# Performance work log

Hardware: AMD Instinct MI355X
Metric: run time of the kernel (lower is better)

## Reference

```python
import jax, jax.numpy as jnp
import numpy as np

B, S, L, H, E, V = 32, 48, 48, 1024, 1024, 32000


def setup_inputs() -> dict:
    key = jax.random.key(0)
    ks = jax.random.split(key, 16)
    s = 0.02
    return {
        "label": jax.random.randint(ks[0], (B, S), 0, V),
        "init_hidden": jax.random.normal(ks[1], (1, B, H), jnp.float32),
        "encoder_output": jax.random.normal(ks[2], (B, L, H), jnp.float32),
        "emb": jax.random.normal(ks[3], (V, E), jnp.float32) * s,
        "attn_W": jax.random.normal(ks[4], (2 * H, L), jnp.float32) * s,
        "attn_b": jnp.zeros((L,), jnp.float32),
        "comb_W": jax.random.normal(ks[5], (2 * H, H), jnp.float32) * s,
        "comb_b": jnp.zeros((H,), jnp.float32),
        "W_ih": jax.random.normal(ks[6], (E, 3 * H), jnp.float32) * s,
        "W_hh": jax.random.normal(ks[7], (H, 3 * H), jnp.float32) * s,
        "b_ih": jnp.zeros((3 * H,), jnp.float32),
        "b_hh": jnp.zeros((3 * H,), jnp.float32),
        "out_W": jax.random.normal(ks[8], (H, V), jnp.float32) * s,
        "out_b": jnp.zeros((V,), jnp.float32),
    }


def _decode(label, init_hidden, encoder_output, emb, attn_W, attn_b,
            comb_W, comb_b, W_ih, W_hh, b_ih, b_hh, out_W, out_b):
    # Teacher forcing (teaching_force_rate=1.0): inputs are relu(embedding(label[:, i]))
    xs = jax.nn.relu(emb[label])            # (B, S, E)
    xs = jnp.transpose(xs, (1, 0, 2))       # (S, B, E) for scan

    def step(h, xe):                        # h: (B,H), xe: (B,E)
        # Attention: Linear(cat(emb, hidden)) -> nn.Softmax() on a 3D (B,1,L)
        # tensor, which in torch defaults to dim=0 (the batch dim) -- replicated.
        sim = jnp.concatenate([xe, h], axis=-1) @ attn_W + attn_b   # (B, L)
        w = jax.nn.softmax(sim, axis=0)                             # over batch (faithful)
        ctx = jnp.einsum('bl,blh->bh', w, encoder_output)           # bmm
        g = jax.nn.relu(jnp.concatenate([ctx, xe], axis=-1) @ comb_W + comb_b)  # (B,H)
        # Single GRU step (torch gate order: r, z, n)
        gx = g @ W_ih + b_ih
        gh = h @ W_hh + b_hh
        xr, xz, xn = jnp.split(gx, 3, axis=-1)
        hr, hz, hn = jnp.split(gh, 3, axis=-1)
        r = jax.nn.sigmoid(xr + hr)
        z = jax.nn.sigmoid(xz + hz)
        n = jnp.tanh(xn + r * hn)
        h_new = (1.0 - z) * n + z * h
        out = jax.nn.log_softmax(h_new @ out_W + out_b, axis=-1)    # (B, V)
        return h_new, out

    _, outs = jax.lax.scan(step, init_hidden[0], xs)   # outs: (S, B, V)
    return jnp.transpose(outs, (1, 0, 2))              # (B, S, V)


def reference(label, init_hidden, encoder_output, emb, attn_W, attn_b,
              comb_W, comb_b, W_ih, W_hh, b_ih, b_hh, out_W, out_b):
    return _decode(label, init_hidden, encoder_output, emb, attn_W, attn_b,
                   comb_W, comb_b, W_ih, W_hh, b_ih, b_hh, out_W, out_b)
```

## Files before the change

### kernel.cpp

```cpp
#include <hip/hip_runtime.h>

#define NB 32
#define NS 48
#define NL 48
#define NH 1024
#define NE 1024
#define NV 32000
#define NR (NS*NB)
#define K3H 3072
#define RA_BLOCKS 64
#define RB_BLOCKS 128
#define RC_BLOCKS 64
#define NBLK_FULL (RA_BLOCKS + RB_BLOCKS + RC_BLOCKS)

typedef unsigned short u16;
typedef __bf16 bf16x8 __attribute__((ext_vector_type(8)));
typedef unsigned short ushort8 __attribute__((ext_vector_type(8)));
typedef float f32x4 __attribute__((ext_vector_type(4)));
typedef unsigned int uint4v __attribute__((ext_vector_type(4)));

__device__ __forceinline__ float bf2f(u16 x) {
    union { unsigned u; float f; } c; c.u = ((unsigned)x) << 16; return c.f;
}
__device__ __forceinline__ u16 f2bf(float f) {
    union { float f; unsigned u; } c; c.f = f;
    unsigned r = (c.u + 0x7FFFu + ((c.u >> 16) & 1u)) >> 16;
    return (u16)r;
}
__device__ __forceinline__ f32x4 mfma16(bf16x8 a, bf16x8 b, f32x4 c) {
    return __builtin_amdgcn_mfma_f32_16x16x32_bf16(a, b, c, 0, 0, 0);
}
__device__ __forceinline__ void gld_lds16(const void* g, void* l) {
    __builtin_amdgcn_global_load_lds((const __attribute__((address_space(1))) void*)g,
                                     (__attribute__((address_space(3))) void*)l, 16, 0, 0);
}

__device__ __forceinline__ void st16_coh(void* p, uint4v v) {
    asm volatile("global_store_dwordx4 %0, %1, off sc0 sc1" :: "v"(p), "v"(v) : "memory");
}
__device__ __forceinline__ void waitb(const int* line, int tgt) {
    if (tgt <= 0) return;
    int guard = 0; int v;
    for (;;) {
        asm volatile("global_load_dword %0, %1, off sc0 sc1\n\ts_waitcnt vmcnt(0)"
                     : "=v"(v) : "v"(line) : "memory");
        if (v >= tgt) return;
        __builtin_amdgcn_s_sleep(1);
        if (++guard > (1 << 20)) return;
    }
}
__device__ __forceinline__ void arrive2(int* cnt, int* superc, int* bcast, int lineMask, int val) {
    asm volatile("s_waitcnt vmcnt(0)" ::: "memory");
    int prev = __hip_atomic_fetch_add(cnt, 1, __ATOMIC_RELAXED, __HIP_MEMORY_SCOPE_AGENT);
    if ((prev & lineMask) == lineMask) {
        int p2 = __hip_atomic_fetch_add(superc, 1, __ATOMIC_RELAXED, __HIP_MEMORY_SCOPE_AGENT);
        if ((p2 & 7) == 7) {
#pragma unroll
            for (int i = 0; i < 24; ++i)
                asm volatile("global_store_dword %0, %1, off sc0 sc1"
                             :: "v"(bcast + i * 64), "v"(val) : "memory");
        }
    }
}

__global__ __launch_bounds__(256) void transpose_cast(const float* __restrict__ src, int K, int N,
                                                      char* __restrict__ dst, int bf16out) {
    __shared__ float tile[32][33];
    int k0 = blockIdx.y * 32, n0 = blockIdx.x * 32;
    int tx = threadIdx.x & 31, ty = threadIdx.x >> 5;
    for (int i = 0; i < 4; ++i) {
        int n = n0 + tx;
        float v = (n < N) ? src[(size_t)(k0 + ty + i*8) * N + n] : 0.f;
        tile[ty + i*8][tx] = v;
    }
    __syncthreads();
    for (int i = 0; i < 4; ++i) {
        int n = n0 + ty + i*8;
        int k = k0 + tx;
        if (n < N) {
            float v = tile[tx][ty + i*8];
            if (bf16out) ((u16*)dst)[(size_t)n * K + k] = f2bf(v);
            else         ((float*)dst)[(size_t)n * K + k] = v;
        }
    }
}

__global__ __launch_bounds__(256) void prep_inputs(const int* __restrict__ label, const float* __restrict__ emb,
                                                   const float* __restrict__ enc, const float* __restrict__ inith,
                                                   u16* __restrict__ xe, u16* __restrict__ encb, u16* __restrict__ hallx) {
    int blk = blockIdx.x, t = threadIdx.x;
    if (blk < NR) {
        int s = blk >> 5, b = blk & 31;
        int lab = label[b * NS + s];
        const float* src = emb + (size_t)lab * NE;
        u16* dst = xe + (size_t)blk * NE;
        for (int i = t; i < NE; i += 256) { float v = src[i]; dst[i] = f2bf(v > 0.f ? v : 0.f); }
    } else if (blk < 2 * NR) {
        int r = blk - NR;
        const float* src = enc + (size_t)r * NH;
        u16* dst = encb + (size_t)r * NH;
        for (int i = t; i < NH; i += 256) dst[i] = f2bf(src[i]);
    } else {
        int b = blk - 2 * NR;
        const float* src = inith + (size_t)b * NH;
        u16* dst = hallx + (size_t)b * NH;
        for (int i = t; i < NH; i += 256) dst[i] = f2bf(src[i]);
    }
}

__global__ __launch_bounds__(384) void simxe2_kernel(const u16* __restrict__ xe, const u16* __restrict__ aw1t,
                                                     const float* __restrict__ attnB, float* __restrict__ simxe) {
    int r = blockIdx.x, t = threadIdx.x;
    int l = t >> 3, part = t & 7;
    const u16* x = xe + (size_t)r * 1024 + part * 128;
    const u16* ww = aw1t + (size_t)l * 1024 + part * 128;
    float acc = 0.f;
#pragma unroll
    for (int k = 0; k < 128; k += 8) {
        ushort8 xv = *reinterpret_cast<const ushort8*>(x + k);
        ushort8 wv = *reinterpret_cast<const ushort8*>(ww + k);
#pragma unroll
        for (int u = 0; u < 8; ++u) acc += bf2f(xv[u]) * bf2f(wv[u]);
    }
    acc += __shfl_xor(acc, 1);
    acc += __shfl_xor(acc, 2);
    acc += __shfl_xor(acc, 4);
    if (part == 0) simxe[(size_t)r * NL + l] = acc + attnB[l];
}

template<int MODE>
__global__ __launch_bounds__(256) void gemm_bf16(const u16* __restrict__ A, const u16* __restrict__ Bt,
                                                 void* __restrict__ Cout, const float* __restrict__ bias, int N) {
    __shared__ u16 ldsA[128 * 64];
    __shared__ u16 ldsB[128 * 64];
    const int t = threadIdx.x;
    const int lane = t & 63, w = t >> 6;
    const int wm = w >> 1, wn = w & 1;
    const int m0 = blockIdx.x * 128, n0 = blockIdx.y * 128;
    f32x4 acc[4][4] = {};
    for (int kt = 0; kt < 16; ++kt) {
        const int k0 = kt * 64;
#pragma unroll
        for (int i = 0; i < 4; ++i) {
            int chunk = i * 256 + t;
            int row = chunk >> 3, slot = chunk & 7;
            int srck = ((slot ^ (row & 7)) * 8);
            const u16* ga = A  + (size_t)(m0 + row) * 1024 + k0 + srck;
            const u16* gb = Bt + (size_t)(n0 + row) * 1024 + k0 + srck;
            u16* la = ldsA + (size_t)(i * 256 + w * 64) * 8;
            u16* lb = ldsB + (size_t)(i * 256 + w * 64) * 8;
            gld_lds16(ga, la);
            gld_lds16(gb, lb);
        }
        asm volatile("s_waitcnt vmcnt(0)" ::: "memory");
        __syncthreads();
#pragma unroll
        for (int kk = 0; kk < 2; ++kk) {
            bf16x8 a[4], b[4];
#pragma unroll
            for (int f = 0; f < 4; ++f) {
                int rowA = wm * 64 + f * 16 + (lane & 15);
                int slotA = (kk * 4 + (lane >> 4)) ^ (rowA & 7);
                a[f] = *reinterpret_cast<const bf16x8*>(ldsA + rowA * 64 + slotA * 8);
                int rowB = wn * 64 + f * 16 + (lane & 15);
                int slotB = (kk * 4 + (lane >> 4)) ^ (rowB & 7);
                b[f] = *reinterpret_cast<const bf16x8*>(ldsB + rowB * 64 + slotB * 8);
            }
#pragma unroll
            for (int fm = 0; fm < 4; ++fm)
#pragma unroll
                for (int fn = 0; fn < 4; ++fn)
                    acc[fm][fn] = mfma16(a[fm], b[fn], acc[fm][fn]);
        }
        __syncthreads();
    }
#pragma unroll
    for (int fm = 0; fm < 4; ++fm) {
#pragma unroll
        for (int fn = 0; fn < 4; ++fn) {
#pragma unroll
            for (int rr = 0; rr < 4; ++rr) {
                int m = m0 + wm * 64 + fm * 16 + (lane >> 4) * 4 + rr;
                int n = n0 + wn * 64 + fn * 16 + (lane & 15);
                float v = acc[fm][fn][rr];
                if (bias) v += bias[n];
                if (MODE == 0)      ((float*)Cout)[(size_t)m * N + n] = v;
                else if (MODE == 2) ((u16*)Cout)[(size_t)m * N + n] = f2bf(v);
                else if (MODE == 1)
                    ((float*)Cout)[((size_t)(m & 31) * NS + (m >> 5)) * NV + n] = v;
                else
                    ((u16*)Cout)[((size_t)(m & 31) * NS + (m >> 5)) * NV + n] = f2bf(v);
            }
        }
    }
}

__device__ __forceinline__ void do_tile256(char* smem, const u16* Ab, const u16* outWT,
                                           const float* outB, u16* logit,
                                           int mt, int nt, int t) {
    u16* ldsA = (u16*)smem;
    u16* ldsB = (u16*)(smem + 32768);
    const int w = t >> 6, lane = t & 63;
    const int r16 = lane & 15, kg = lane >> 4;
    const int wm = w >> 1, wn = w & 1;
    const int m0 = mt * 256, n0 = nt * 128;
    f32x4 acc[4][4] = {};
    for (int kt = 0; kt < 16; ++kt) {
        const int k0 = kt * 64;
#pragma unroll
        for (int i = 0; i < 4; ++i) {
            int chunk = i * 512 + t;
            int row = chunk >> 3, slot = chunk & 7;
            int srck = ((slot ^ (row & 7)) * 8);
            gld_lds16(Ab + (size_t)(m0 + row) * 1024 + k0 + srck,
                      ldsA + (size_t)(i * 512 + w * 64) * 8);
        }
#pragma unroll
        for (int i = 0; i < 2; ++i) {
            int chunk = i * 512 + t;
            int row = chunk >> 3, slot = chunk & 7;
            int srck = ((slot ^ (row & 7)) * 8);
            gld_lds16(outWT + (size_t)(n0 + row) * 1024 + k0 + srck,
                      ldsB + (size_t)(i * 512 + w * 64) * 8);
        }
        asm volatile("s_waitcnt vmcnt(0)" ::: "memory");
        __syncthreads();
#pragma unroll
        for (int kk = 0; kk < 2; ++kk) {
            bf16x8 a[4], b[4];
#pragma unroll
            for (int f = 0; f < 4; ++f) {
                int rowA = wm * 64 + f * 16 + r16;
                int slotA = (kk * 4 + kg) ^ (rowA & 7);
                a[f] = *reinterpret_cast<const bf16x8*>(ldsA + rowA * 64 + slotA * 8);
                int rowB = wn * 64 + f * 16 + r16;
                int slotB = (kk * 4 + kg) ^ (rowB & 7);
                b[f] = *reinterpret_cast<const bf16x8*>(ldsB + rowB * 64 + slotB * 8);
            }
#pragma unroll
            for (int fm = 0; fm < 4; ++fm)
#pragma unroll
                for (int fn = 0; fn < 4; ++fn)
                    acc[fm][fn] = mfma16(a[fm], b[fn], acc[fm][fn]);
        }
        __syncthreads();
    }
#pragma unroll
    for (int fm = 0; fm < 4; ++fm) {
#pragma unroll
        for (int fn = 0; fn < 4; ++fn) {
#pragma unroll
            for (int rr = 0; rr < 4; ++rr) {
                int m = m0 + wm * 64 + fm * 16 + kg * 4 + rr;
                int n = n0 + wn * 64 + fn * 16 + r16;
                float v = acc[fm][fn][rr] + outB[n];
                logit[((size_t)(m & 31) * NS + (m >> 5)) * NV + n] = f2bf(v);
            }
        }
    }
}

__device__ __forceinline__ void queue_gemm(char* smem, int* qslot, int* qcnt,
                                           const u16* Ab, const u16* outWT,
                                           const float* outB, u16* logit, int t) {
    for (;;) {
        __syncthreads();
        if (t == 0) *qslot = __hip_atomic_fetch_add(qcnt, 1, __ATOMIC_RELAXED, __HIP_MEMORY_SCOPE_AGENT);
        __syncthreads();
        int nt = *qslot;
        if (nt >= 250) return;
        do_tile256(smem, Ab, outWT, outB, logit, 5, nt, t);
    }
}

__global__ __launch_bounds__(512) void recurrence9(
    const float* __restrict__ simxe, const u16* __restrict__ gxe,
    const u16* __restrict__ P, const u16* __restrict__ aw2t,
    const u16* __restrict__ whht, const u16* __restrict__ wiht,
    const float* __restrict__ b_ih, const float* __restrict__ b_hh,
    u16* __restrict__ g_rot, u16* __restrict__ hallx,
    const float* __restrict__ outW, const float* __restrict__ outB,
    u16* __restrict__ outWT, u16* __restrict__ logit, int* __restrict__ bar, int fused)
{
    __shared__ __align__(16) char smem[155776];
    int* cntA   = bar;
    int* cntB   = bar + 512;
    int* superA = bar + 1024;
    int* superB = bar + 1088;
    int* bcastA = bar + 1152;
    int* bcastB = bar + 2688;
    int* cntC   = bar + 4224;
    int* qcnt   = bar + 4288;
    int* qslot  = (int*)(smem + 153600);
    const int blk = blockIdx.x, t = threadIdx.x;
    const int lane = t & 63, w = t >> 6;
    const int r16 = lane & 15, kg = lane >> 4;
    const u16* Ab = hallx + NB * NH;

    if (blk < RA_BLOCKS) {
        int* myB = bcastB + (blk % 24) * 64;
        const int b = blk >> 1, half = blk & 1;
        u16*   W2T  = (u16*)smem;
        u16*   Pl   = (u16*)(smem + 99072);
        float* siml = (float*)(smem + 148224);
        float* wl   = (float*)(smem + 154496);
        u16*   gtmp = (u16*)(smem + 154752);
        for (int idx = t; idx < 48 * 1024; idx += 512) {
            int l = idx >> 10, k = idx & 1023;
            W2T[l * 1032 + k] = aw2t[idx];
        }
        for (int idx = t; idx < 48 * 512; idx += 512) {
            int l = idx >> 9, j = idx & 511;
            Pl[idx] = P[((size_t)(b * 48 + l)) * NH + half * 512 + j];
        }
        __syncthreads();
        const int mt = w & 1, nt = w >> 1;
        const int m0 = mt * 16, n0 = nt * 16;

        for (int s = 0; s < NS; ++s) {
            float gxev = bf2f(gxe[((size_t)(s * 32 + b)) * NH + half * 512 + t]);
            float sxv0 = 0.f, sxv1 = 0.f, sxv2 = 0.f, sxv3 = 0.f;
            if (w < 6) {
                const float* sxe = simxe + (size_t)(s * 32) * NL;
                sxv0 = sxe[(m0 + kg * 4 + 0) * NL + n0 + r16];
                sxv1 = sxe[(m0 + kg * 4 + 1) * NL + n0 + r16];
                sxv2 = sxe[(m0 + kg * 4 + 2) * NL + n0 + r16];
                sxv3 = sxe[(m0 + kg * 4 + 3) * NL + n0 + r16];
            }
            if (t == 0) waitb(myB, s);
            __syncthreads();
            const u16* hprev = hallx + (size_t)s * (NB * NH);
            if (w < 6) {
                f32x4 acc0; f32x4 acc1 = {};
                acc0[0] = sxv0; acc0[1] = sxv1; acc0[2] = sxv2; acc0[3] = sxv3;
                const u16* aP = hprev + (size_t)(m0 + r16) * NH + kg * 8;
                const u16* bP = W2T + (n0 + r16) * 1032 + kg * 8;
#pragma unroll
                for (int k = 0; k < 1024; k += 64) {
                    acc0 = mfma16(*reinterpret_cast<const bf16x8*>(aP + k),
                                  *reinterpret_cast<const bf16x8*>(bP + k), acc0);
                    acc1 = mfma16(*reinterpret_cast<const bf16x8*>(aP + k + 32),
                                  *reinterpret_cast<const bf16x8*>(bP + k + 32), acc1);
                }
#pragma unroll
                for (int rr = 0; rr < 4; ++rr)
                    siml[(m0 + kg * 4 + rr) * 49 + n0 + r16] = acc0[rr] + acc1[rr];
            }
            __syncthreads();
            if (t < 384) {
                int l = t >> 3, p = t & 7;
                float v0 = siml[(p * 4 + 0) * 49 + l];
                float v1 = siml[(p * 4 + 1) * 49 + l];
                float v2 = siml[(p * 4 + 2) * 49 + l];
                float v3 = siml[(p * 4 + 3) * 49 + l];
                float m = fmaxf(fmaxf(v0, v1), fmaxf(v2, v3));
                m = fmaxf(m, __shfl_xor(m, 1));
                m = fmaxf(m, __shfl_xor(m, 2));
                m = fmaxf(m, __shfl_xor(m, 4));
                float den = __expf(v0 - m) + __expf(v1 - m) + __expf(v2 - m) + __expf(v3 - m);
                den += __shfl_xor(den, 1);
                den += __shfl_xor(den, 2);
                den += __shfl_xor(den, 4);
                if (p == (b >> 2)) {
                    int bi = b & 3;
                    float vb = bi == 0 ? v0 : bi == 1 ? v1 : bi == 2 ? v2 : v3;
                    wl[l] = __expf(vb - m) / den;
                }
            }
            __syncthreads();
            {
                float acc = gxev;
#pragma unroll
                for (int l = 0; l < 48; ++l) acc += wl[l] * bf2f(Pl[l * 512 + t]);
                gtmp[t] = f2bf(fmaxf(acc, 0.f));
            }
            __syncthreads();
            if (t < 64) {
                uint4v v = *reinterpret_cast<const uint4v*>(gtmp + t * 8);
                st16_coh(g_rot + (size_t)s * (NB * NH) + (size_t)b * NH + half * 512 + t * 8, v);
            }
            if (t == 0) arrive2(cntA + (blk & 7) * 64, superA, bcastA, 7, s + 1);
        }
        if (fused) {
            if (t == 0) { waitb(myB, 48); waitb(cntC, RC_BLOCKS); }
            __syncthreads();
            queue_gemm(smem, qslot, qcnt, Ab, outWT, outB, logit, t);
        }
    } else if (blk < RA_BLOCKS + RB_BLOCKS) {
        const int rb = blk - RA_BLOCKS;
        int* myB = bcastB + (rb % 24) * 64;
        int* myA = bcastA + (rb % 24) * 64;
        const int c0 = rb * 8;
        u16*   Whh = (u16*)smem;
        u16*   Wih = (u16*)(smem + 66048);
        float* ghs = (float*)(smem + 132096);
        float* gxs = (float*)(smem + 140288);
        u16*   htmp = (u16*)(smem + 148480);
        for (int idx = t; idx < 32 * 1024; idx += 512) {
            int pr = idx >> 10, k = idx & 1023;
            u16 vh = 0, vi = 0;
            if (pr < 24) {
                size_t srow = (size_t)((pr >> 3) * 1024 + c0 + (pr & 7));
                vh = whht[srow * NH + k];
                vi = wiht[srow * NH + k];
            }
            Whh[pr * 1032 + k] = vh;
            Wih[pr * 1032 + k] = vi;
        }
        const int gb2 = (t & 255) >> 3, gcol = t & 7;
        const float bxr = b_ih[c0 + gcol], bxz = b_ih[1024 + c0 + gcol], bxn = b_ih[2048 + c0 + gcol];
        const float bhr = b_hh[c0 + gcol], bhz = b_hh[1024 + c0 + gcol], bhn = b_hh[2048 + c0 + gcol];
        __syncthreads();
        const int mt = (w >> 1) & 1, nt = w & 1, kh = w >> 2;
        const int m0 = mt * 16;

        for (int s = 0; s < NS; ++s) {
            if (t == 0) waitb(myB, s);
            __syncthreads();
            const u16* hprev = hallx + (size_t)s * (NB * NH);
            const u16* gcur  = g_rot + (size_t)s * (NB * NH);
            float hold = bf2f(hprev[(size_t)gb2 * NH + c0 + gcol]);
            {
                f32x4 acc0 = {}, acc1 = {};
                const u16* aP = hprev + (size_t)(m0 + r16) * NH + kh * 512 + kg * 8;
                const u16* bP = Whh + (nt * 16 + r16) * 1032 + kh * 512 + kg * 8;
#pragma unroll
                for (int k = 0; k < 512; k += 64) {
                    acc0 = mfma16(*reinterpret_cast<const bf16x8*>(aP + k),
                                  *reinterpret_cast<const bf16x8*>(bP + k), acc0);
                    acc1 = mfma16(*reinterpret_cast<const bf16x8*>(aP + k + 32),
                                  *reinterpret_cast<const bf16x8*>(bP + k + 32), acc1);
                }
#pragma unroll
                for (int rr = 0; rr < 4; ++rr)
                    ghs[kh * 1024 + (m0 + kg * 4 + rr) * 32 + nt * 16 + r16] = acc0[rr] + acc1[rr];
            }
            if (t == 0) waitb(myA, s + 1);
            __syncthreads();
            {
                f32x4 acc0 = {}, acc1 = {};
                const u16* aP = gcur + (size_t)(m0 + r16) * NH + kh * 512 + kg * 8;
                const u16* bP = Wih + (nt * 16 + r16) * 1032 + kh * 512 + kg * 8;
#pragma unroll
                for (int k = 0; k < 512; k += 64) {
                    acc0 = mfma16(*reinterpret_cast<const bf16x8*>(aP + k),
                                  *reinterpret_cast<const bf16x8*>(bP + k), acc0);
                    acc1 = mfma16(*reinterpret_cast<const bf16x8*>(aP + k + 32),
                                  *reinterpret_cast<const bf16x8*>(bP + k + 32), acc1);
                }
#pragma unroll
                for (int rr = 0; rr < 4; ++rr)
                    gxs[kh * 1024 + (m0 + kg * 4 + rr) * 32 + nt * 16 + r16] = acc0[rr] + acc1[rr];
            }
            __syncthreads();
            if (t < 256) {
                float gxr = gxs[gb2 * 32 + gcol]      + gxs[1024 + gb2 * 32 + gcol]      + bxr;
                float gxz = gxs[gb2 * 32 + 8 + gcol]  + gxs[1024 + gb2 * 32 + 8 + gcol]  + bxz;
                float gxn = gxs[gb2 * 32 + 16 + gcol] + gxs[1024 + gb2 * 32 + 16 + gcol] + bxn;
                float ghr = ghs[gb2 * 32 + gcol]      + ghs[1024 + gb2 * 32 + gcol]      + bhr;
                float ghz = ghs[gb2 * 32 + 8 + gcol]  + ghs[1024 + gb2 * 32 + 8 + gcol]  + bhz;
                float ghn = ghs[gb2 * 32 + 16 + gcol] + ghs[1024 + gb2 * 32 + 16 + gcol] + bhn;
                float rg = 1.f / (1.f + __expf(-(gxr + ghr)));
                float zg = 1.f / (1.f + __expf(-(gxz + ghz)));
                float ng = tanhf(gxn + rg * ghn);
                float hnew = (1.f - zg) * ng + zg * hold;
                htmp[t] = f2bf(hnew);
            }
            __syncthreads();
            if (t < 32) {
                uint4v v = *reinterpret_cast<const uint4v*>(htmp + t * 8);
                st16_coh(hallx + ((size_t)(s + 1) * NB + t) * NH + c0, v);
            }
            if (t == 0) arrive2(cntB + (rb & 7) * 64, superB, bcastB, 15, s + 1);
        }
        if (fused) {
            if (t == 0) { waitb(myB, 48); waitb(cntC, RC_BLOCKS); }
            __syncthreads();
            queue_gemm(smem, qslot, qcnt, Ab, outWT, outB, logit, t);
        }
    } else {
        const int rc = blk - (RA_BLOCKS + RB_BLOCKS);
        {
            float* ttile = (float*)smem;
            const int sub = t >> 7, u = t & 127;
            for (int T0 = 0; T0 < 32000; T0 += 256) {
                int T = T0 + rc * 4 + sub;
                int tn = T >> 5, tk = T & 31;
                int n0 = tn * 32, k0 = tk * 32;
                __syncthreads();
#pragma unroll
                for (int j = 0; j < 8; ++j) {
                    int e = j * 128 + u;
                    int row = e >> 5, col = e & 31;
                    ttile[(sub * 32 + row) * 33 + col] = outW[(size_t)(k0 + row) * NV + n0 + col];
                }
                __syncthreads();
                int nr = u >> 2, kc = u & 3;
                unsigned pk0, pk1, pk2, pk3;
                {
                    const float* base = ttile + (sub * 32 + kc * 8) * 33 + nr;
                    pk0 = (unsigned)f2bf(base[0])   | ((unsigned)f2bf(base[33])  << 16);
                    pk1 = (unsigned)f2bf(base[66])  | ((unsigned)f2bf(base[99])  << 16);
                    pk2 = (unsigned)f2bf(base[132]) | ((unsigned)f2bf(base[165]) << 16);
                    pk3 = (unsigned)f2bf(base[198]) | ((unsigned)f2bf(base[231]) << 16);
                }
                uint4v v; v[0] = pk0; v[1] = pk1; v[2] = pk2; v[3] = pk3;
                st16_coh(outWT + (size_t)(n0 + nr) * NH + k0 + kc * 8, v);
            }
            asm volatile("s_waitcnt vmcnt(0)" ::: "memory");
            __syncthreads();
            if (t == 0) {
                __hip_atomic_fetch_add(cntC, 1, __ATOMIC_RELAXED, __HIP_MEMORY_SCOPE_AGENT);
                waitb(cntC, RC_BLOCKS);
            }
            __syncthreads();
        }
        int lastReady = 0;
        for (int T = rc; T < 1250; T += RC_BLOCKS) {
            int mt = T / 250, nt = T - mt * 250;
            int need = 8 * mt + 8;
            if (need > lastReady) {
                if (t == 0) waitb(bcastB + (rc % 24) * 64, need);
                lastReady = need;
            }
            __syncthreads();
            do_tile256(smem, Ab, outWT, outB, logit, mt, nt, t);
        }
        if (t == 0) waitb(bcastB + (rc % 24) * 64, 48);
        __syncthreads();
        queue_gemm(smem, qslot, qcnt, Ab, outWT, outB, logit, t);
    }
}

__global__ __launch_bounds__(256) void logsoftmax_kernel(float* __restrict__ out) {
    __shared__ float red[8];
    float* row = out + (size_t)blockIdx.x * NV;
    int t = threadIdx.x;
    float m = -1e30f;
    for (int i = t; i < NV; i += 256) m = fmaxf(m, row[i]);
    for (int o = 32; o >= 1; o >>= 1) m = fmaxf(m, __shfl_xor(m, o));
    if ((t & 63) == 0) red[t >> 6] = m;
    __syncthreads();
    m = fmaxf(fmaxf(red[0], red[1]), fmaxf(red[2], red[3]));
    float sum = 0.f;
    for (int i = t; i < NV; i += 256) sum += __expf(row[i] - m);
    for (int o = 32; o >= 1; o >>= 1) sum += __shfl_xor(sum, o);
    if ((t & 63) == 0) red[4 + (t >> 6)] = sum;
    __syncthreads();
    sum = (red[4] + red[5]) + (red[6] + red[7]);
    float lse = m + __logf(sum);
    for (int i = t; i < NV; i += 256) row[i] = row[i] - lse;
}

__global__ __launch_bounds__(1024) void logsoftmax_bf16(const u16* __restrict__ lg, float* __restrict__ out) {
    __shared__ __align__(16) u16 rowb[NV];
    __shared__ float red[32];
    const u16* src = lg + (size_t)blockIdx.x * NV;
    float* dst = out + (size_t)blockIdx.x * NV;
    int t = threadIdx.x;
    for (int i = t; i < NV / 8; i += 1024)
        ((ushort8*)rowb)[i] = ((const ushort8*)src)[i];
    __syncthreads();
    float m = -1e30f;
    for (int i = t; i < NV; i += 1024) m = fmaxf(m, bf2f(rowb[i]));
    for (int o = 32; o >= 1; o >>= 1) m = fmaxf(m, __shfl_xor(m, o));
    if ((t & 63) == 0) red[t >> 6] = m;
    __syncthreads();
    m = red[0];
#pragma unroll
    for (int i = 1; i < 16; ++i) m = fmaxf(m, red[i]);
    float sum = 0.f;
    for (int i = t; i < NV; i += 1024) sum += __expf(bf2f(rowb[i]) - m);
    for (int o = 32; o >= 1; o >>= 1) sum += __shfl_xor(sum, o);
    if ((t & 63) == 0) red[16 + (t >> 6)] = sum;
    __syncthreads();
    sum = 0.f;
#pragma unroll
    for (int i = 0; i < 16; ++i) sum += red[16 + i];
    float lse = m + __logf(sum);
    for (int i = t; i < NV; i += 1024) dst[i] = bf2f(rowb[i]) - lse;
}

extern "C" void kernel_launch(void* const* d_in, const int* in_sizes, int n_in,
                              void* d_out, int out_size, void* d_ws, size_t ws_size,
                              hipStream_t stream) {
    const int*   label = (const int*)  d_in[0];
    const float* inith = (const float*)d_in[1];
    const float* enc   = (const float*)d_in[2];
    const float* emb   = (const float*)d_in[3];
    const float* attnW = (const float*)d_in[4];
    const float* attnB = (const float*)d_in[5];
    const float* combW = (const float*)d_in[6];
    const float* combB = (const float*)d_in[7];
    const float* Wih   = (const float*)d_in[8];
    const float* Whh   = (const float*)d_in[9];
    const float* bih   = (const float*)d_in[10];
    const float* bhh   = (const float*)d_in[11];
    const float* outW  = (const float*)d_in[12];
    const float* outB  = (const float*)d_in[13];
    char* ws = (char*)d_ws;

    size_t BAR_OFF    = 0;
    size_t OUTWT_OFF  = 32768;
    size_t WHHT_OFF   = OUTWT_OFF + (size_t)NV*NH*2;
    size_t WIHT_OFF   = WHHT_OFF + (size_t)K3H*NH*2;
    size_t CW1T_OFF   = WIHT_OFF + (size_t)K3H*NH*2;
    size_t CW2T_OFF   = CW1T_OFF + (size_t)NH*NH*2;
    size_t AW2T_OFF   = CW2T_OFF + (size_t)NH*NH*2;
    size_t AW1T_OFF   = AW2T_OFF + (size_t)NL*NH*2;
    size_t XE_OFF     = AW2T_OFF + (size_t)NL*NH*4;
    size_t ENCB_OFF   = XE_OFF   + (size_t)NR*NE*2;
    size_t SIMXE_OFF  = ENCB_OFF + (size_t)NR*NH*2;
    size_t GXE_OFF    = SIMXE_OFF+ (size_t)NR*NL*4;
    size_t P_OFF      = GXE_OFF  + (size_t)NR*NH*2;
    size_t HALL_OFF   = P_OFF    + (size_t)NR*NH*2;
    size_t GROT_OFF   = HALL_OFF + (size_t)(NS+1)*NB*NH*2;
    size_t LOGIT_OFF  = GROT_OFF + (size_t)NS*NB*NH*2;
    size_t TOTAL_NEED = LOGIT_OFF+ (size_t)NR*NV*2;

    int*   bar   = (int*)(ws + BAR_OFF);
    u16*   outWT = (u16*)(ws + OUTWT_OFF);
    u16*   whht  = (u16*)(ws + WHHT_OFF);
    u16*   wiht  = (u16*)(ws + WIHT_OFF);
    u16*   cw1t  = (u16*)(ws + CW1T_OFF);
    u16*   cw2t  = (u16*)(ws + CW2T_OFF);
    u16*   aw2t  = (u16*)(ws + AW2T_OFF);
    u16*   aw1t  = (u16*)(ws + AW1T_OFF);
    u16*   xe    = (u16*)(ws + XE_OFF);
    u16*   encb  = (u16*)(ws + ENCB_OFF);
    float* simxe = (float*)(ws + SIMXE_OFF);
    u16*   gxe   = (u16*)(ws + GXE_OFF);
    u16*   Pb    = (u16*)(ws + P_OFF);
    u16*   hallx = (u16*)(ws + HALL_OFF);
    u16*   grot  = (u16*)(ws + GROT_OFF);
    u16*   logit = (u16*)(ws + LOGIT_OFF);

    hipMemsetAsync(bar, 0, 32768, stream);
    prep_inputs<<<2 * NR + NB, 256, 0, stream>>>(label, emb, enc, inith, xe, encb, hallx);

    transpose_cast<<<dim3(K3H / 32, 32), 256, 0, stream>>>(Whh, NH, K3H, (char*)whht, 1);
    transpose_cast<<<dim3(K3H / 32, 32), 256, 0, stream>>>(Wih, NH, K3H, (char*)wiht, 1);
    transpose_cast<<<dim3(NH / 32, 32), 256, 0, stream>>>(combW, NH, NH, (char*)cw1t, 1);
    transpose_cast<<<dim3(NH / 32, 32), 256, 0, stream>>>(combW + (size_t)NH * NH, NH, NH, (char*)cw2t, 1);
    transpose_cast<<<dim3(2, 32), 256, 0, stream>>>(attnW + (size_t)NH * NL, NH, NL, (char*)aw2t, 1);
    transpose_cast<<<dim3(2, 32), 256, 0, stream>>>(attnW, NH, NL, (char*)aw1t, 1);

    simxe2_kernel<<<NR, 384, 0, stream>>>(xe, aw1t, attnB, simxe);
    gemm_bf16<2><<<dim3(NR / 128, NH / 128), 256, 0, stream>>>(xe, cw2t, gxe, combB, NH);
    gemm_bf16<2><<<dim3(NR / 128, NH / 128), 256, 0, stream>>>(encb, cw1t, Pb, nullptr, NH);

    if (ws_size >= TOTAL_NEED) {
        recurrence9<<<NBLK_FULL, 512, 0, stream>>>(simxe, gxe, Pb, aw2t, whht, wiht,
                                                   bih, bhh, grot, hallx,
                                                   outW, outB, outWT, logit, bar, 1);
        logsoftmax_bf16<<<NR, 1024, 0, stream>>>(logit, (float*)d_out);
    } else {
        transpose_cast<<<dim3(NV / 32, 32), 256, 0, stream>>>(outW, NH, NV, (char*)outWT, 1);
        recurrence9<<<RA_BLOCKS + RB_BLOCKS, 512, 0, stream>>>(simxe, gxe, Pb, aw2t, whht, wiht,
                                                               bih, bhh, grot, hallx,
                                                               outW, outB, outWT, logit, bar, 0);
        gemm_bf16<1><<<dim3(NR / 128, NV / 128), 256, 0, stream>>>(hallx + (size_t)NB * NH, outWT, d_out, outB, NV);
        logsoftmax_kernel<<<NR, 256, 0, stream>>>((float*)d_out);
    }
}
```

Measured before the change: 922.9 us.

## Widen output-projection tiles to 256x256 and batch prologue launches

The vocab projection tile inside the persistent recurrence kernel grows from 256x128 to 256x256, halving the tile count and doubling per-wave accumulators, so each A tile loaded to LDS is reused across more output columns. The six weight transposes are merged into one launch, and the two prologue GEMMs into one launch via blockIdx.z, to cut launch overhead. The larger tile raises register pressure (4x8 accumulators per wave) and coarsens load balance across the 64 consumer blocks.

Result: faster. 900.7 us (-2.4%).

```diff
diff --git a/kernel.cpp b/kernel.cpp
--- a/kernel.cpp
+++ b/kernel.cpp
@@ -82,6 +82,36 @@
             if (bf16out) ((u16*)dst)[(size_t)n * K + k] = f2bf(v);
             else         ((float*)dst)[(size_t)n * K + k] = v;
         }
+    }
+}
+
+__global__ __launch_bounds__(256) void transpose_all(const float* __restrict__ Whh_, const float* __restrict__ Wih_,
+                                                     const float* __restrict__ combW_, const float* __restrict__ attnW_,
+                                                     u16* __restrict__ whht, u16* __restrict__ wiht,
+                                                     u16* __restrict__ cw1t, u16* __restrict__ cw2t,
+                                                     u16* __restrict__ aw2t, u16* __restrict__ aw1t) {
+    __shared__ float tile[32][33];
+    int bid = blockIdx.x;
+    const float* src; u16* dst; int N, local;
+    if (bid < 3072)      { src = Whh_;  dst = whht; N = 3072; local = bid; }
+    else if (bid < 6144) { src = Wih_;  dst = wiht; N = 3072; local = bid - 3072; }
+    else if (bid < 7168) { src = combW_; dst = cw1t; N = 1024; local = bid - 6144; }
+    else if (bid < 8192) { src = combW_ + (size_t)NH * NH; dst = cw2t; N = 1024; local = bid - 7168; }
+    else if (bid < 8256) { src = attnW_ + (size_t)NH * NL; dst = aw2t; N = 48; local = bid - 8192; }
+    else                 { src = attnW_; dst = aw1t; N = 48; local = bid - 8256; }
+    int tiles_x = (N + 31) >> 5;
+    int n0 = (local % tiles_x) * 32, k0 = (local / tiles_x) * 32;
+    int tx = threadIdx.x & 31, ty = threadIdx.x >> 5;
+    for (int i = 0; i < 4; ++i) {
+        int n = n0 + tx;
+        float v = (n < N) ? src[(size_t)(k0 + ty + i*8) * N + n] : 0.f;
+        tile[ty + i*8][tx] = v;
+    }
+    __syncthreads();
+    for (int i = 0; i < 4; ++i) {
+        int n = n0 + ty + i*8;
+        int k = k0 + tx;
+        if (n < N) dst[(size_t)n * 1024 + k] = f2bf(tile[tx][ty + i*8]);
     }
 }
 
@@ -145,12 +175,8 @@
             int chunk = i * 256 + t;
             int row = chunk >> 3, slot = chunk & 7;
             int srck = ((slot ^ (row & 7)) * 8);
-            const u16* ga = A  + (size_t)(m0 + row) * 1024 + k0 + srck;
-            const u16* gb = Bt + (size_t)(n0 + row) * 1024 + k0 + srck;
-            u16* la = ldsA + (size_t)(i * 256 + w * 64) * 8;
-            u16* lb = ldsB + (size_t)(i * 256 + w * 64) * 8;
-            gld_lds16(ga, la);
-            gld_lds16(gb, lb);
+            gld_lds16(A  + (size_t)(m0 + row) * 1024 + k0 + srck, ldsA + (size_t)(i * 256 + w * 64) * 8);
+            gld_lds16(Bt + (size_t)(n0 + row) * 1024 + k0 + srck, ldsB + (size_t)(i * 256 + w * 64) * 8);
         }
         asm volatile("s_waitcnt vmcnt(0)" ::: "memory");
         __syncthreads();
@@ -195,16 +221,78 @@
     }
 }
 
-__device__ __forceinline__ void do_tile256(char* smem, const u16* Ab, const u16* outWT,
-                                           const float* outB, u16* logit,
-                                           int mt, int nt, int t) {
+__global__ __launch_bounds__(256) void gemm_pro(const u16* __restrict__ xe, const u16* __restrict__ cw2t,
+                                                const u16* __restrict__ encb, const u16* __restrict__ cw1t,
+                                                u16* __restrict__ gxe, u16* __restrict__ Pb,
+                                                const float* __restrict__ combB) {
+    __shared__ u16 ldsA[128 * 64];
+    __shared__ u16 ldsB[128 * 64];
+    const u16 *A, *Bt; u16* C; const float* bias;
+    if (blockIdx.z == 0) { A = xe;   Bt = cw2t; C = gxe; bias = combB; }
+    else                 { A = encb; Bt = cw1t; C = Pb;  bias = nullptr; }
+    const int t = threadIdx.x;
+    const int lane = t & 63, w = t >> 6;
+    const int wm = w >> 1, wn = w & 1;
+    const int m0 = blockIdx.x * 128, n0 = blockIdx.y * 128;
+    f32x4 acc[4][4] = {};
+    for (int kt = 0; kt < 16; ++kt) {
+        const int k0 = kt * 64;
+#pragma unroll
+        for (int i = 0; i < 4; ++i) {
+            int chunk = i * 256 + t;
+            int row = chunk >> 3, slot = chunk & 7;
+            int srck = ((slot ^ (row & 7)) * 8);
+            gld_lds16(A  + (size_t)(m0 + row) * 1024 + k0 + srck, ldsA + (size_t)(i * 256 + w * 64) * 8);
+            gld_lds16(Bt + (size_t)(n0 + row) * 1024 + k0 + srck, ldsB + (size_t)(i * 256 + w * 64) * 8);
+        }
+        asm volatile("s_waitcnt vmcnt(0)" ::: "memory");
+        __syncthreads();
+#pragma unroll
+        for (int kk = 0; kk < 2; ++kk) {
+            bf16x8 a[4], b[4];
+#pragma unroll
+            for (int f = 0; f < 4; ++f) {
+                int rowA = wm * 64 + f * 16 + (lane & 15);
+                int slotA = (kk * 4 + (lane >> 4)) ^ (rowA & 7);
+                a[f] = *reinterpret_cast<const bf16x8*>(ldsA + rowA * 64 + slotA * 8);
+                int rowB = wn * 64 + f * 16 + (lane & 15);
+                int slotB = (kk * 4 + (lane >> 4)) ^ (rowB & 7);
+                b[f] = *reinterpret_cast<const bf16x8*>(ldsB + rowB * 64 + slotB * 8);
+            }
+#pragma unroll
+            for (int fm = 0; fm < 4; ++fm)
+#pragma unroll
+                for (int fn = 0; fn < 4; ++fn)
+                    acc[fm][fn] = mfma16(a[fm], b[fn], acc[fm][fn]);
+        }
+        __syncthreads();
+    }
+#pragma unroll
+    for (int fm = 0; fm < 4; ++fm) {
+#pragma unroll
+        for (int fn = 0; fn < 4; ++fn) {
+#pragma unroll
+            for (int rr = 0; rr < 4; ++rr) {
+                int m = m0 + wm * 64 + fm * 16 + (lane >> 4) * 4 + rr;
+                int n = n0 + wn * 64 + fn * 16 + (lane & 15);
+                float v = acc[fm][fn][rr];
+                if (bias) v += bias[n];
+                C[(size_t)m * NH + n] = f2bf(v);
+            }
+        }
+    }
+}
+
+__device__ __forceinline__ void do_tile(char* smem, const u16* Ab, const u16* outWT,
+                                        const float* outB, u16* logit,
+                                        int mt, int nt, int t) {
     u16* ldsA = (u16*)smem;
     u16* ldsB = (u16*)(smem + 32768);
     const int w = t >> 6, lane = t & 63;
     const int r16 = lane & 15, kg = lane >> 4;
     const int wm = w >> 1, wn = w & 1;
-    const int m0 = mt * 256, n0 = nt * 128;
-    f32x4 acc[4][4] = {};
+    const int m0 = mt * 256, n0 = nt * 256;
+    f32x4 acc[4][8] = {};
     for (int kt = 0; kt < 16; ++kt) {
         const int k0 = kt * 64;
 #pragma unroll
@@ -214,12 +302,6 @@
             int srck = ((slot ^ (row & 7)) * 8);
             gld_lds16(Ab + (size_t)(m0 + row) * 1024 + k0 + srck,
                       ldsA + (size_t)(i * 512 + w * 64) * 8);
-        }
-#pragma unroll
-        for (int i = 0; i < 2; ++i) {
-            int chunk = i * 512 + t;
-            int row = chunk >> 3, slot = chunk & 7;
-            int srck = ((slot ^ (row & 7)) * 8);
             gld_lds16(outWT + (size_t)(n0 + row) * 1024 + k0 + srck,
                       ldsB + (size_t)(i * 512 + w * 64) * 8);
         }
@@ -227,20 +309,23 @@
         __syncthreads();
 #pragma unroll
         for (int kk = 0; kk < 2; ++kk) {
-            bf16x8 a[4], b[4];
+            bf16x8 a[4], b[8];
 #pragma unroll
             for (int f = 0; f < 4; ++f) {
                 int rowA = wm * 64 + f * 16 + r16;
                 int slotA = (kk * 4 + kg) ^ (rowA & 7);
                 a[f] = *reinterpret_cast<const bf16x8*>(ldsA + rowA * 64 + slotA * 8);
-                int rowB = wn * 64 + f * 16 + r16;
+            }
+#pragma unroll
+            for (int f = 0; f < 8; ++f) {
+                int rowB = wn * 128 + f * 16 + r16;
                 int slotB = (kk * 4 + kg) ^ (rowB & 7);
                 b[f] = *reinterpret_cast<const bf16x8*>(ldsB + rowB * 64 + slotB * 8);
             }
 #pragma unroll
             for (int fm = 0; fm < 4; ++fm)
 #pragma unroll
-                for (int fn = 0; fn < 4; ++fn)
+                for (int fn = 0; fn < 8; ++fn)
                     acc[fm][fn] = mfma16(a[fm], b[fn], acc[fm][fn]);
         }
         __syncthreads();
@@ -248,11 +333,11 @@
 #pragma unroll
     for (int fm = 0; fm < 4; ++fm) {
 #pragma unroll
-        for (int fn = 0; fn < 4; ++fn) {
+        for (int fn = 0; fn < 8; ++fn) {
 #pragma unroll
             for (int rr = 0; rr < 4; ++rr) {
                 int m = m0 + wm * 64 + fm * 16 + kg * 4 + rr;
-                int n = n0 + wn * 64 + fn * 16 + r16;
+                int n = n0 + wn * 128 + fn * 16 + r16;
                 float v = acc[fm][fn][rr] + outB[n];
                 logit[((size_t)(m & 31) * NS + (m >> 5)) * NV + n] = f2bf(v);
             }
@@ -268,12 +353,12 @@
         if (t == 0) *qslot = __hip_atomic_fetch_add(qcnt, 1, __ATOMIC_RELAXED, __HIP_MEMORY_SCOPE_AGENT);
         __syncthreads();
         int nt = *qslot;
-        if (nt >= 250) return;
-        do_tile256(smem, Ab, outWT, outB, logit, 5, nt, t);
-    }
-}
-
-__global__ __launch_bounds__(512) void recurrence9(
+        if (nt >= 125) return;
+        do_tile(smem, Ab, outWT, outB, logit, 5, nt, t);
+    }
+}
+
+__global__ __launch_bounds__(512) void recurrence10(
     const float* __restrict__ simxe, const u16* __restrict__ gxe,
     const u16* __restrict__ P, const u16* __restrict__ aw2t,
     const u16* __restrict__ whht, const u16* __restrict__ wiht,
@@ -516,15 +601,15 @@
             __syncthreads();
         }
         int lastReady = 0;
-        for (int T = rc; T < 1250; T += RC_BLOCKS) {
-            int mt = T / 250, nt = T - mt * 250;
+        for (int T = rc; T < 625; T += RC_BLOCKS) {
+            int mt = T / 125, nt = T - mt * 125;
             int need = 8 * mt + 8;
             if (need > lastReady) {
                 if (t == 0) waitb(bcastB + (rc % 24) * 64, need);
                 lastReady = need;
             }
             __syncthreads();
-            do_tile256(smem, Ab, outWT, outB, logit, mt, nt, t);
+            do_tile(smem, Ab, outWT, outB, logit, mt, nt, t);
         }
         if (t == 0) waitb(bcastB + (rc % 24) * 64, 48);
         __syncthreads();
@@ -638,27 +723,22 @@
     hipMemsetAsync(bar, 0, 32768, stream);
     prep_inputs<<<2 * NR + NB, 256, 0, stream>>>(label, emb, enc, inith, xe, encb, hallx);
 
-    transpose_cast<<<dim3(K3H / 32, 32), 256, 0, stream>>>(Whh, NH, K3H, (char*)whht, 1);
-    transpose_cast<<<dim3(K3H / 32, 32), 256, 0, stream>>>(Wih, NH, K3H, (char*)wiht, 1);
-    transpose_cast<<<dim3(NH / 32, 32), 256, 0, stream>>>(combW, NH, NH, (char*)cw1t, 1);
-    transpose_cast<<<dim3(NH / 32, 32), 256, 0, stream>>>(combW + (size_t)NH * NH, NH, NH, (char*)cw2t, 1);
-    transpose_cast<<<dim3(2, 32), 256, 0, stream>>>(attnW + (size_t)NH * NL, NH, NL, (char*)aw2t, 1);
-    transpose_cast<<<dim3(2, 32), 256, 0, stream>>>(attnW, NH, NL, (char*)aw1t, 1);
+    transpose_all<<<8320, 256, 0, stream>>>(Whh, Wih, combW, attnW,
+                                            whht, wiht, cw1t, cw2t, aw2t, aw1t);
 
     simxe2_kernel<<<NR, 384, 0, stream>>>(xe, aw1t, attnB, simxe);
-    gemm_bf16<2><<<dim3(NR / 128, NH / 128), 256, 0, stream>>>(xe, cw2t, gxe, combB, NH);
-    gemm_bf16<2><<<dim3(NR / 128, NH / 128), 256, 0, stream>>>(encb, cw1t, Pb, nullptr, NH);
+    gemm_pro<<<dim3(NR / 128, NH / 128, 2), 256, 0, stream>>>(xe, cw2t, encb, cw1t, gxe, Pb, combB);
 
     if (ws_size >= TOTAL_NEED) {
-        recurrence9<<<NBLK_FULL, 512, 0, stream>>>(simxe, gxe, Pb, aw2t, whht, wiht,
-                                                   bih, bhh, grot, hallx,
-                                                   outW, outB, outWT, logit, bar, 1);
+        recurrence10<<<NBLK_FULL, 512, 0, stream>>>(simxe, gxe, Pb, aw2t, whht, wiht,
+                                                    bih, bhh, grot, hallx,
+                                                    outW, outB, outWT, logit, bar, 1);
         logsoftmax_bf16<<<NR, 1024, 0, stream>>>(logit, (float*)d_out);
     } else {
         transpose_cast<<<dim3(NV / 32, 32), 256, 0, stream>>>(outW, NH, NV, (char*)outWT, 1);
-        recurrence9<<<RA_BLOCKS + RB_BLOCKS, 512, 0, stream>>>(simxe, gxe, Pb, aw2t, whht, wiht,
-                                                               bih, bhh, grot, hallx,
-                                                               outW, outB, outWT, logit, bar, 0);
+        recurrence10<<<RA_BLOCKS + RB_BLOCKS, 512, 0, stream>>>(simxe, gxe, Pb, aw2t, whht, wiht,
+                                                                bih, bhh, grot, hallx,
+                                                                outW, outB, outWT, logit, bar, 0);
         gemm_bf16<1><<<dim3(NR / 128, NV / 128), 256, 0, stream>>>(hallx + (size_t)NB * NH, outWT, d_out, outB, NV);
         logsoftmax_kernel<<<NR, 256, 0, stream>>>((float*)d_out);
     }
```
